# Kernel optimization log

Measured on AMD Instinct MI355X. Metric: run time of the kernel, lower is better.

Reference implementation:

```python
import jax, jax.numpy as jnp
import numpy as np

SOFTCAP = 50.0
EPS = 1e-6
N_HEADS, D_HEAD = 16, 64


def _rms(x, w):
    return x * jax.lax.rsqrt(jnp.mean(x * x, axis=-1, keepdims=True) + EPS) * w


def _rope(x, cos, sin):
    # Faithful to source: apply_rope uses x.size(1) as the position axis, but is
    # called on (B, H, T, Dh) tensors, so positions are indexed by HEAD index.
    n = x.shape[1]
    x1, x2 = x[..., 0::2], x[..., 1::2]
    c = cos[:n][None, :, None, :]
    s = sin[:n][None, :, None, :]
    return jnp.stack([x1 * c - x2 * s, x1 * s + x2 * c], axis=-1).reshape(x.shape)


def setup_inputs() -> dict:
    key = jax.random.key(0)
    ks = jax.random.split(key, 12)
    L, D, H, Dh, Dff, V, B, T = 6, 1024, N_HEADS, D_HEAD, 4096, 32000, 1, 1024
    r = lambda k, shape: jax.random.normal(k, shape, dtype=jnp.float32) * 0.02
    return {
        'x': jax.random.randint(ks[0], (B, T), 0, V, dtype=jnp.int32),
        'embed': r(ks[1], (V, D)),
        'ln1': jnp.ones((L, D), jnp.float32),
        'Wq': r(ks[2], (L, H * Dh, D)),
        'Wk': r(ks[3], (L, H * Dh, D)),
        'Wv': r(ks[4], (L, H * Dh, D)),
        'Wo': r(ks[5], (L, D, H * Dh)),
        'qn': jnp.ones((L, Dh), jnp.float32),
        'kn': jnp.ones((L, Dh), jnp.float32),
        'ln2': jnp.ones((L, D), jnp.float32),
        'Wg': r(ks[6], (L, Dff, D)),
        'Wu': r(ks[7], (L, Dff, D)),
        'Wd': r(ks[8], (L, D, Dff)),
        'ln_out': jnp.ones((D,), jnp.float32),
    }


def reference(x, embed, ln1, Wq, Wk, Wv, Wo, qn, kn, ln2, Wg, Wu, Wd, ln_out):
    B, T = x.shape
    H, Dh = N_HEADS, D_HEAD
    scale = Dh ** -0.5
    # RoPE tables (theta=10000)
    freqs = 1.0 / (10000.0 ** (jnp.arange(0, Dh, 2, dtype=jnp.float32) / Dh))
    ang = jnp.arange(T, dtype=jnp.float32)[:, None] * freqs[None, :]
    cos, sin = jnp.cos(ang), jnp.sin(ang)
    mask = jnp.triu(jnp.ones((T, T), dtype=bool), k=1)  # True above diagonal

    h = embed[x]  # (B, T, D)

    def block(h, p):
        l1, wq, wk, wv, wo, qnw, knw, l2, wg, wu, wd = p
        hn = _rms(h, l1)
        q = (hn @ wq.T).reshape(B, T, H, Dh).transpose(0, 2, 1, 3)  # (B,H,T,Dh)
        k = (hn @ wk.T).reshape(B, T, H, Dh).transpose(0, 2, 1, 3)
        v = (hn @ wv.T).reshape(B, T, H, Dh).transpose(0, 2, 1, 3)
        q = _rope(_rms(q, qnw), cos, sin)
        k = _rope(_rms(k, knw), cos, sin)
        scores = jnp.einsum('bhtd,bhsd->bhts', q, k) * scale
        scores = SOFTCAP * jnp.tanh(scores / SOFTCAP)
        scores = jnp.where(mask[None, None], -jnp.inf, scores)
        attn = jax.nn.softmax(scores, axis=-1)
        o = jnp.einsum('bhts,bhsd->bhtd', attn, v)
        o = o.transpose(0, 2, 1, 3).reshape(B, T, H * Dh)
        h = h + o @ wo.T
        hn2 = _rms(h, l2)
        h = h + (jax.nn.silu(hn2 @ wg.T) * (hn2 @ wu.T)) @ wd.T
        return h, None

    h, _ = jax.lax.scan(block, h, (ln1, Wq, Wk, Wv, Wo, qn, kn, ln2, Wg, Wu, Wd))
    # tied embed/head
    logits = _rms(h, ln_out) @ embed.T  # (B, T, V)
    return logits
```

## Files before the change

### kernel.cpp

```cpp
#include <hip/hip_runtime.h>
#include <math.h>
#include <type_traits>

typedef __bf16 bf16_t;
typedef bf16_t bf16x4 __attribute__((ext_vector_type(4)));
typedef bf16_t bf16x8 __attribute__((ext_vector_type(8)));
typedef float  f32x4  __attribute__((ext_vector_type(4)));

#define RMS_EPS 1e-6f

enum { EP_STORE = 0, EP_RESID = 1, EP_SPLIT = 2, EP_SILU = 3, EP_QKV = 4 };

template<int V> using IC = std::integral_constant<int, V>;

static __device__ __forceinline__ f32x4 mfma16(bf16x8 a, bf16x8 b, f32x4 c) {
    return __builtin_amdgcn_mfma_f32_16x16x32_bf16(a, b, c, 0, 0, 0);
}

#define GLDS(gp, lp) __builtin_amdgcn_global_load_lds( \
    (const __attribute__((address_space(1))) void*)(gp), \
    (__attribute__((address_space(3))) void*)(lp), 16, 0, 0)

template<int N> static __device__ __forceinline__ void vmwait() {
    if constexpr (N == 0)      asm volatile("s_waitcnt vmcnt(0)" ::: "memory");
    else if constexpr (N == 2) asm volatile("s_waitcnt vmcnt(2)" ::: "memory");
    else if constexpr (N == 3) asm volatile("s_waitcnt vmcnt(3)" ::: "memory");
    else if constexpr (N == 4) asm volatile("s_waitcnt vmcnt(4)" ::: "memory");
    else if constexpr (N == 6) asm volatile("s_waitcnt vmcnt(6)" ::: "memory");
    else if constexpr (N == 8) asm volatile("s_waitcnt vmcnt(8)" ::: "memory");
    __builtin_amdgcn_sched_barrier(0);
}
static __device__ __forceinline__ void bar() { __builtin_amdgcn_s_barrier(); }
static __device__ __forceinline__ void lgkm0() {
    asm volatile("s_waitcnt lgkmcnt(0)" ::: "memory");
    __builtin_amdgcn_sched_barrier(0);
}

template<int BM, int BN, int WR, int WC, int PLANES, int EPIL, int MINW, int DEPTH>
__global__ __launch_bounds__(WR * WC * 64, MINW)
void gemm_bf16(const bf16_t* __restrict__ Ah, const bf16_t* __restrict__ Al,
               const bf16_t* __restrict__ Bh,
               float* __restrict__ Cf, bf16_t* __restrict__ Ch, bf16_t* __restrict__ Cl,
               int K, int lda, int ldb, int ldc, long long sC,
               const float* __restrict__ qnw, const float* __restrict__ knw)
{
    constexpr int ASZ = BM * 32, BSZ = BN * 32;
    constexpr int NW = WR * WC;
    constexpr int NLD = (BM / 16 * (PLANES >= 2 ? 2 : 1) + BN / 16) / NW;
    __shared__ __align__(16) bf16_t sAh[DEPTH][ASZ], sBh[DEPTH][BSZ];
    __shared__ __align__(16) bf16_t sAl[PLANES >= 2 ? DEPTH : 1][PLANES >= 2 ? ASZ : 8];

    const int gx = gridDim.x;
    int id = blockIdx.x + gx * blockIdx.y;
    if (gridDim.z == 1) {
        int nwg = gx * gridDim.y;
        int q = nwg >> 3, r = nwg & 7;
        int xcd = id & 7, ix = id >> 3;
        id = (xcd < r ? xcd * (q + 1) : r * (q + 1) + (xcd - r) * q) + ix;
    }
    const int bm = id % gx, bn = id / gx;
    const int row0 = bm * BM, col0 = bn * BN;

    const size_t kofs = (size_t)blockIdx.z * K;
    Ah += kofs;  Bh += kofs;
    if constexpr (PLANES >= 2) Al += kofs;

    const int tid = threadIdx.x, lane = tid & 63, wave = tid >> 6;
    const int lr = lane & 15, lg = lane >> 4;
    constexpr int WM = BM / WR, WN = BN / WC, MF = WM / 16, NF = WN / 16;
    const int wr = wave / WC, wc = wave % WC;

    f32x4 acc[MF][NF];
    #pragma unroll
    for (int m = 0; m < MF; ++m)
        #pragma unroll
        for (int n = 0; n < NF; ++n) acc[m][n] = (f32x4){0.f, 0.f, 0.f, 0.f};

    auto stage = [&](int k0, int p) {
        #pragma unroll
        for (int i = wave; i < BM / 16; i += NW) {
            int s = i * 64 + lane, rr = s >> 2, c = s & 3;
            size_t go = (size_t)(row0 + rr) * lda + k0 + ((c ^ ((rr >> 1) & 3)) << 3);
            GLDS(Ah + go, &sAh[p][i * 512]);
            if constexpr (PLANES >= 2) GLDS(Al + go, &sAl[p][i * 512]);
        }
        #pragma unroll
        for (int i = wave; i < BN / 16; i += NW) {
            int s = i * 64 + lane, rr = s >> 2, c = s & 3;
            size_t go = (size_t)(col0 + rr) * ldb + k0 + ((c ^ ((rr >> 1) & 3)) << 3);
            GLDS(Bh + go, &sBh[p][i * 512]);
        }
    };

    auto compute = [&](int p) {
        bf16x8 ahf[MF], alf[MF], bhf[NF];
        #pragma unroll
        for (int m = 0; m < MF; ++m) {
            int rr = wr * WM + m * 16 + lr;
            int by = rr * 64 + ((lg ^ ((rr >> 1) & 3)) << 4);
            ahf[m] = *(const bf16x8*)((const char*)&sAh[p][0] + by);
            if constexpr (PLANES >= 2)
                alf[m] = *(const bf16x8*)((const char*)&sAl[p][0] + by);
        }
        #pragma unroll
        for (int n = 0; n < NF; ++n) {
            int rr = wc * WN + n * 16 + lr;
            int by = rr * 64 + ((lg ^ ((rr >> 1) & 3)) << 4);
            bhf[n] = *(const bf16x8*)((const char*)&sBh[p][0] + by);
        }
        #pragma unroll
        for (int m = 0; m < MF; ++m)
            #pragma unroll
            for (int n = 0; n < NF; ++n) {
                acc[m][n] = mfma16(ahf[m], bhf[n], acc[m][n]);
                if constexpr (PLANES >= 2)
                    acc[m][n] = mfma16(alf[m], bhf[n], acc[m][n]);
            }
    };

    if constexpr (DEPTH == 3) {
        const int NC = K >> 5;
        stage(0, 0);
        stage(32, 1);
        for (int j = 0; j + 2 < NC; ++j) {
            stage(32 * (j + 2), (j + 2) % 3);
            vmwait<2 * NLD>(); bar();
            compute(j % 3);
            bar();
        }
        vmwait<NLD>(); bar();
        compute((K >> 5) >= 2 ? ((K >> 5) - 2) % 3 : 0);
        vmwait<0>(); bar();
        compute(((K >> 5) - 1) % 3);
    } else {
        stage(0, 0);
        int k0 = 32;
        for (; k0 + 32 < K; k0 += 64) {
            stage(k0, 1);
            vmwait<NLD>(); bar();
            compute(0);
            bar();
            stage(k0 + 32, 0);
            vmwait<NLD>(); bar();
            compute(1);
            bar();
        }
        stage(k0, 1);
        vmwait<NLD>(); bar();
        compute(0);
        bar();
        vmwait<0>(); bar();
        compute(1);
    }

    if constexpr (EPIL == EP_QKV) {
        const int colbase = col0 + wc * WN;
        const int typ = colbase >> 10;
        if (typ < 2) {
            const float* nw = (typ == 0) ? qnw : knw;
            const int hh = (colbase - typ * 1024) >> 6;
            constexpr float kLogF = -0.41524101186092029f;
            #pragma unroll
            for (int m = 0; m < MF; ++m)
                #pragma unroll
                for (int r = 0; r < 4; ++r) {
                    int grow = row0 + wr * WM + m * 16 + lg * 4 + r;
                    float ss = 0.f;
                    #pragma unroll
                    for (int n = 0; n < NF; ++n) {
                        float v = acc[m][n][r];
                        ss += v * v;
                    }
                    ss += __shfl_xor(ss, 1, 64);
                    ss += __shfl_xor(ss, 2, 64);
                    ss += __shfl_xor(ss, 4, 64);
                    ss += __shfl_xor(ss, 8, 64);
                    float inv = rsqrtf(ss * (1.0f / 64.0f) + RMS_EPS);
                    #pragma unroll
                    for (int n = 0; n < NF; ++n) {
                        int i = n * 16 + lr;
                        float x = acc[m][n][r] * inv * nw[i];
                        float p = __shfl_xor(x, 1, 64);
                        float f = exp2f((float)(i >> 1) * kLogF);
                        float ang = (float)hh * f;
                        float cs = cosf(ang), sn = sinf(ang);
                        float o = (lr & 1) ? (p * sn + x * cs) : (x * cs - p * sn);
                        Ch[(size_t)grow * ldc + colbase + i] = (bf16_t)o;
                    }
                }
        } else {
            bf16_t* vTh_ = Cl;
            bf16_t* vTl_ = (bf16_t*)Cf;
            const int vcb = colbase - 2048;
            #pragma unroll
            for (int m = 0; m < MF; ++m)
                #pragma unroll
                for (int n = 0; n < NF; ++n) {
                    int vc = vcb + n * 16 + lr;
                    int grow0 = row0 + wr * WM + m * 16 + lg * 4;
                    bf16x4 hv, lv;
                    #pragma unroll
                    for (int r = 0; r < 4; ++r) {
                        float v = acc[m][n][r];
                        bf16_t hb = (bf16_t)v;
                        hv[r] = hb;
                        lv[r] = (bf16_t)(v - (float)hb);
                    }
                    *(bf16x4*)&vTh_[(size_t)vc * 1024 + grow0] = hv;
                    *(bf16x4*)&vTl_[(size_t)vc * 1024 + grow0] = lv;
                }
        }
        return;
    }

    #pragma unroll
    for (int m = 0; m < MF; ++m)
        #pragma unroll
        for (int n = 0; n < NF; ++n)
            #pragma unroll
            for (int r = 0; r < 4; ++r) {
                int grow = row0 + wr * WM + m * 16 + lg * 4 + r;
                int gcol = col0 + wc * WN + n * 16 + lr;
                float v = acc[m][n][r];
                if constexpr (EPIL == EP_SILU) {
                    float pv = __shfl_xor(v, 1, 64);
                    if (!(lr & 1)) {
                        float s = (v / (1.0f + __expf(-v))) * pv;
                        size_t off = (size_t)grow * ldc + (gcol >> 1);
                        Ch[off] = (bf16_t)s;
                    }
                } else {
                    size_t off = (size_t)blockIdx.z * sC + (size_t)grow * ldc + gcol;
                    if constexpr (EPIL == EP_STORE) {
                        Cf[off] = v;
                    } else if constexpr (EPIL == EP_RESID) {
                        Cf[off] += v;
                    } else {
                        bf16_t hb = (bf16_t)v;
                        Ch[off] = hb;
                        Cl[off] = (bf16_t)(v - (float)hb);
                    }
                }
            }
}

__global__ __launch_bounds__(512, 2)
void gemm_logits8(const bf16_t* __restrict__ Ah, const bf16_t* __restrict__ Bh,
                  float* __restrict__ Cf)
{
    constexpr int lda = 1024, ldb = 1024, ldc = 32000;
    constexpr int NT = 16;
    __shared__ __align__(16) bf16_t sA[2][2][256 * 32];
    __shared__ __align__(16) bf16_t sB[2][2][256 * 32];

    const int gx = gridDim.x;
    int id = blockIdx.x + gx * blockIdx.y;
    {
        int nwg = gx * gridDim.y;
        int q = nwg >> 3, r = nwg & 7;
        int xcd = id & 7, ix = id >> 3;
        id = (xcd < r ? xcd * (q + 1) : r * (q + 1) + (xcd - r) * q) + ix;
    }
    const int bm = id % gx, bn = id / gx;
    const int row0 = bm * 256, col0 = bn * 256;

    const int tid = threadIdx.x, lane = tid & 63, wave = tid >> 6;
    const int lr = lane & 15, lg = lane >> 4;
    const int wr = wave >> 2, wc = wave & 3;

    f32x4 acc[8][4];
    #pragma unroll
    for (int m = 0; m < 8; ++m)
        #pragma unroll
        for (int n = 0; n < 4; ++n) acc[m][n] = (f32x4){0.f, 0.f, 0.f, 0.f};

    auto stageA = [&](int chunk, int buf, int ks) {
        int k0 = chunk * 32;
        #pragma unroll
        for (int i = wave; i < 16; i += 8) {
            int s = i * 64 + lane, rr = s >> 2, c = s & 3;
            size_t go = (size_t)(row0 + rr) * lda + k0 + ((c ^ ((rr >> 1) & 3)) << 3);
            GLDS(Ah + go, &sA[buf][ks][i * 512]);
        }
    };
    auto stageB = [&](int chunk, int buf, int ks) {
        int k0 = chunk * 32;
        #pragma unroll
        for (int i = wave; i < 16; i += 8) {
            int s = i * 64 + lane, rr = s >> 2, c = s & 3;
            size_t go = (size_t)(col0 + rr) * ldb + k0 + ((c ^ ((rr >> 1) & 3)) << 3);
            GLDS(Bh + go, &sB[buf][ks][i * 512]);
        }
    };

    auto phase = [&](int t, auto ksc) {
        constexpr int ks = decltype(ksc)::value;
        const int buf = t & 1;
        bf16x8 af[8], bf4[4];
        #pragma unroll
        for (int m = 0; m < 8; ++m) {
            int rr = wr * 128 + m * 16 + lr;
            int by = rr * 64 + ((lg ^ ((rr >> 1) & 3)) << 4);
            af[m] = *(const bf16x8*)((const char*)&sA[buf][ks][0] + by);
        }
        #pragma unroll
        for (int n = 0; n < 4; ++n) {
            int rr = wc * 64 + n * 16 + lr;
            int by = rr * 64 + ((lg ^ ((rr >> 1) & 3)) << 4);
            bf4[n] = *(const bf16x8*)((const char*)&sB[buf][ks][0] + by);
        }
        if constexpr (ks == 0) {
            if (t + 1 < NT) {
                stageA(2 * (t + 1) + 1, (t + 1) & 1, 1);
                stageB(2 * (t + 1) + 1, (t + 1) & 1, 1);
                vmwait<8>();
            } else {
                vmwait<0>();
            }
        } else {
            if (t + 2 < NT) {
                stageA(2 * (t + 2), t & 1, 0);
                stageB(2 * (t + 2), t & 1, 0);
                vmwait<8>();
            } else if (t + 1 < NT) {
                vmwait<4>();
            } else {
                vmwait<0>();
            }
        }
        bar();
        lgkm0();
        __builtin_amdgcn_s_setprio(1);
        #pragma unroll
        for (int m = 0; m < 8; ++m)
            #pragma unroll
            for (int n = 0; n < 4; ++n)
                acc[m][n] = mfma16(af[m], bf4[n], acc[m][n]);
        __builtin_amdgcn_s_setprio(0);
        bar();
    };

    stageA(0, 0, 0); stageB(0, 0, 0);
    stageA(1, 0, 1); stageB(1, 0, 1);
    stageA(2, 1, 0); stageB(2, 1, 0);
    vmwait<8>(); bar();

    for (int t = 0; t < NT; ++t) {
        phase(t, IC<0>{});
        phase(t, IC<1>{});
    }

    #pragma unroll
    for (int m = 0; m < 8; ++m)
        #pragma unroll
        for (int n = 0; n < 4; ++n)
            #pragma unroll
            for (int r = 0; r < 4; ++r) {
                int grow = row0 + wr * 128 + m * 16 + lg * 4 + r;
                int gcol = col0 + wc * 64 + n * 16 + lr;
                Cf[(size_t)grow * ldc + gcol] = acc[m][n][r];
            }
}

static __device__ __forceinline__ void wsplit_body(
    int b2, int tid,
    const float* wq, const float* wk, const float* wv, const float* wo,
    const float* wg, const float* wu, const float* wd,
    bf16_t* wAh, bf16_t* wGUh, bf16_t* wdh)
{
    #pragma unroll
    for (int k = 0; k < 4; ++k) {
        int b = b2 * 4 + k;
        const float* src;
        bf16_t* dst;
        size_t so, doff;
        if (b < 4096) {
            src = b < 1024 ? wq : b < 2048 ? wk : b < 3072 ? wv : wo;
            so = (size_t)(b & 1023) * 256 + tid;
            doff = (size_t)b * 256 + tid;
            dst = wAh;
        } else if (b < 12288) {
            int bb = b - 4096;
            int row = bb < 4096 ? 2 * bb : 2 * (bb - 4096) + 1;
            src = bb < 4096 ? wg : wu;
            so = (size_t)(bb & 4095) * 256 + tid;
            doff = (size_t)row * 256 + tid;
            dst = wGUh;
        } else {
            src = wd;
            so = (size_t)(b - 12288) * 256 + tid;
            doff = so;
            dst = wdh;
        }
        f32x4 v = ((const f32x4*)src)[so];
        bf16x4 hv;
        #pragma unroll
        for (int j = 0; j < 4; ++j) hv[j] = (bf16_t)v[j];
        ((bf16x4*)dst)[doff] = hv;
    }
}

__global__ __launch_bounds__(256)
void reduce_rms_wsplit(const float* __restrict__ p, float* __restrict__ h,
                       const float* __restrict__ w, bf16_t* __restrict__ outh,
                       const float* wq, const float* wk, const float* wv,
                       const float* wo, const float* wg, const float* wu,
                       const float* wd, bf16_t* wAh, bf16_t* wGUh, bf16_t* wdh)
{
    int blk = blockIdx.x, tid = threadIdx.x;
    if (blk >= 1024) {
        if (wq) wsplit_body(blk - 1024, tid, wq, wk, wv, wo, wg, wu, wd,
                            wAh, wGUh, wdh);
        return;
    }
    size_t i = (size_t)blk * 256 + tid;
    const size_t S = (1024 * 1024) / 4;
    f32x4 a = ((const f32x4*)p)[i];
    f32x4 b = ((const f32x4*)p)[i + S];
    f32x4 c = ((const f32x4*)p)[i + 2 * S];
    f32x4 d = ((const f32x4*)p)[i + 3 * S];
    f32x4 hv = ((const f32x4*)h)[i];
    #pragma unroll
    for (int j = 0; j < 4; ++j) hv[j] += (a[j] + b[j]) + (c[j] + d[j]);
    ((f32x4*)h)[i] = hv;

    float ss = hv[0]*hv[0] + hv[1]*hv[1] + hv[2]*hv[2] + hv[3]*hv[3];
    #pragma unroll
    for (int m = 1; m < 64; m <<= 1) ss += __shfl_xor(ss, m, 64);
    __shared__ float red[4];
    if ((tid & 63) == 0) red[tid >> 6] = ss;
    __syncthreads();
    float tot = red[0] + red[1] + red[2] + red[3];
    float inv = rsqrtf(tot * (1.0f / 1024.0f) + RMS_EPS);
    f32x4 wt4 = *(const f32x4*)(w + tid * 4);
    bf16x4 hv4;
    #pragma unroll
    for (int j = 0; j < 4; ++j) hv4[j] = (bf16_t)(hv[j] * inv * wt4[j]);
    ((bf16x4*)outh)[i] = hv4;
}

__global__ __launch_bounds__(256)
void gather_rms_wsplit(const int* __restrict__ ids, const float* __restrict__ embed,
                       const float* __restrict__ w, float* __restrict__ h,
                       bf16_t* __restrict__ outh,
                       const float* wq, const float* wk, const float* wv,
                       const float* wo, const float* wg, const float* wu,
                       const float* wd, bf16_t* wAh, bf16_t* wGUh, bf16_t* wdh,
                       bf16_t* __restrict__ eh)
{
    int blk = blockIdx.x, tid = threadIdx.x;
    if (blk >= 5120) {
        int b2 = blk - 5120;
        #pragma unroll
        for (int k = 0; k < 4; ++k) {
            size_t so = ((size_t)b2 * 4 + k) * 256 + tid;
            f32x4 v = ((const f32x4*)embed)[so];
            bf16x4 hv;
            #pragma unroll
            for (int j = 0; j < 4; ++j) hv[j] = (bf16_t)v[j];
            ((bf16x4*)eh)[so] = hv;
        }
        return;
    }
    if (blk >= 1024) {
        wsplit_body(blk - 1024, tid, wq, wk, wv, wo, wg, wu, wd, wAh, wGUh, wdh);
        return;
    }
    int row = ids[blk];
    f32x4 v = ((const f32x4*)(embed + (size_t)row * 1024))[tid];
    ((f32x4*)(h + (size_t)blk * 1024))[tid] = v;

    float ss = v[0]*v[0] + v[1]*v[1] + v[2]*v[2] + v[3]*v[3];
    #pragma unroll
    for (int m = 1; m < 64; m <<= 1) ss += __shfl_xor(ss, m, 64);
    __shared__ float red[4];
    if ((tid & 63) == 0) red[tid >> 6] = ss;
    __syncthreads();
    float tot = red[0] + red[1] + red[2] + red[3];
    float inv = rsqrtf(tot * (1.0f / 1024.0f) + RMS_EPS);
    f32x4 wt4 = *(const f32x4*)(w + tid * 4);
    bf16x4 hv;
    #pragma unroll
    for (int j = 0; j < 4; ++j) hv[j] = (bf16_t)(v[j] * inv * wt4[j]);
    ((bf16x4*)outh)[(size_t)blk * 256 + tid] = hv;
}

__global__ __launch_bounds__(128, 2)
void flash_attn(const bf16_t* __restrict__ qkvh,
                const bf16_t* __restrict__ vTh, const bf16_t* __restrict__ vTl,
                bf16_t* __restrict__ oh)
{
    __shared__ __align__(16) bf16_t sQ[32*64], sK[64*64], sVh[64*64], sVl[64*64];
    __shared__ __align__(16) bf16_t sPh[32*64], sPl[32*64];

    const int q0 = blockIdx.x * 32;
    const int hh = blockIdx.y;
    const int tid = threadIdx.x, lane = tid & 63, w = tid >> 6;
    const int lr = lane & 15, lg = lane >> 4;

    #pragma unroll
    for (int ii = 0; ii < 2; ++ii) {
        int r0 = w * 16 + ii * 8;
        int r  = r0 + (lane >> 3);
        int i  = lane & 7;
        GLDS(qkvh + (size_t)(q0 + r) * 3072 + hh * 64 + ((i ^ (r & 7)) << 3),
             sQ + r0 * 64);
    }
    __syncthreads();

    bf16x8 qa[2];
    #pragma unroll
    for (int ks = 0; ks < 2; ++ks) {
        int r = w * 16 + lr;
        qa[ks] = *(const bf16x8*)((const char*)sQ + r * 128 +
                                  ((((ks << 2) | lg) ^ (r & 7)) << 4));
    }

    f32x4 o_acc[4];
    #pragma unroll
    for (int n = 0; n < 4; ++n) o_acc[n] = (f32x4){0.f, 0.f, 0.f, 0.f};
    float m_run[4] = {-1e30f, -1e30f, -1e30f, -1e30f};
    float l_run[4] = {0.f, 0.f, 0.f, 0.f};

    const int ntiles = ((q0 + 31) >> 6) + 1;
    for (int t = 0; t < ntiles; ++t) {
        const int kv0 = t * 64;
        #pragma unroll
        for (int ii = 0; ii < 4; ++ii) {
            int r0 = w * 32 + ii * 8;
            int r  = r0 + (lane >> 3);
            int i  = lane & 7;
            GLDS(qkvh + (size_t)(kv0 + r) * 3072 + 1024 + hh * 64 + ((i ^ (r & 7)) << 3),
                 sK + r0 * 64);
            GLDS(vTh + (size_t)(hh * 64 + r) * 1024 + kv0 + ((i ^ (r & 7)) << 3),
                 sVh + r0 * 64);
            GLDS(vTl + (size_t)(hh * 64 + r) * 1024 + kv0 + ((i ^ (r & 7)) << 3),
                 sVl + r0 * 64);
        }
        __syncthreads();

        f32x4 s_acc[4];
        #pragma unroll
        for (int n = 0; n < 4; ++n) s_acc[n] = (f32x4){0.f, 0.f, 0.f, 0.f};
        #pragma unroll
        for (int ks = 0; ks < 2; ++ks)
            #pragma unroll
            for (int n = 0; n < 4; ++n) {
                int r = n * 16 + lr;
                bf16x8 kb = *(const bf16x8*)((const char*)sK + r * 128 +
                                             ((((ks << 2) | lg) ^ (r & 7)) << 4));
                s_acc[n] = mfma16(qa[ks], kb, s_acc[n]);
            }

        #pragma unroll
        for (int j = 0; j < 4; ++j) {
            int qr = q0 + w * 16 + lg * 4 + j;
            float p[4];
            float mx = -1e30f;
            #pragma unroll
            for (int n = 0; n < 4; ++n) {
                float sx = s_acc[n][j] * (0.125f * 0.02f);
                float v = 50.f * (1.f - 2.f / (1.f + __expf(2.f * sx)));
                int key = kv0 + n * 16 + lr;
                if (key > qr) v = -1e30f;
                p[n] = v;
                mx = fmaxf(mx, v);
            }
            #pragma unroll
            for (int m = 1; m < 16; m <<= 1) mx = fmaxf(mx, __shfl_xor(mx, m, 64));
            float mn = fmaxf(m_run[j], mx);
            float ef = __expf(m_run[j] - mn);
            m_run[j] = mn;
            float rs = 0.f;
            #pragma unroll
            for (int n = 0; n < 4; ++n) {
                float e = __expf(p[n] - mn);
                p[n] = e;
                rs += e;
            }
            #pragma unroll
            for (int m = 1; m < 16; m <<= 1) rs += __shfl_xor(rs, m, 64);
            l_run[j] = l_run[j] * ef + rs;
            #pragma unroll
            for (int n = 0; n < 4; ++n) o_acc[n][j] *= ef;
            int r = w * 16 + lg * 4 + j;
            #pragma unroll
            for (int n = 0; n < 4; ++n) {
                int c = n * 16 + lr;
                int byo = r * 128 + ((((c >> 3) ^ (r & 7)) << 4)) + ((c & 7) << 1);
                bf16_t hb = (bf16_t)p[n];
                *(bf16_t*)((char*)sPh + byo) = hb;
                *(bf16_t*)((char*)sPl + byo) = (bf16_t)(p[n] - (float)hb);
            }
        }

        #pragma unroll
        for (int ks = 0; ks < 2; ++ks) {
            int pr = w * 16 + lr;
            int pby = pr * 128 + ((((ks << 2) | lg) ^ (pr & 7)) << 4);
            bf16x8 pa  = *(const bf16x8*)((const char*)sPh + pby);
            bf16x8 pl_ = *(const bf16x8*)((const char*)sPl + pby);
            #pragma unroll
            for (int n = 0; n < 4; ++n) {
                int vr = n * 16 + lr;
                int vby = vr * 128 + ((((ks << 2) | lg) ^ (vr & 7)) << 4);
                bf16x8 vhf = *(const bf16x8*)((const char*)sVh + vby);
                bf16x8 vlf = *(const bf16x8*)((const char*)sVl + vby);
                o_acc[n] = mfma16(pa,  vhf, o_acc[n]);
                o_acc[n] = mfma16(pl_, vhf, o_acc[n]);
                o_acc[n] = mfma16(pa,  vlf, o_acc[n]);
            }
        }
        __syncthreads();
    }

    #pragma unroll
    for (int j = 0; j < 4; ++j) {
        float inv = 1.0f / l_run[j];
        int qr = q0 + w * 16 + lg * 4 + j;
        #pragma unroll
        for (int n = 0; n < 4; ++n) {
            size_t off = (size_t)qr * 1024 + hh * 64 + n * 16 + lr;
            oh[off] = (bf16_t)(o_acc[n][j] * inv);
        }
    }
}

__global__ __launch_bounds__(256)
void rmsnorm_split(const float* __restrict__ in, const float* __restrict__ w,
                   bf16_t* __restrict__ outh)
{
    int row = blockIdx.x, tid = threadIdx.x;
    f32x4 v = *(const f32x4*)(in + (size_t)row * 1024 + tid * 4);
    float ss = v[0]*v[0] + v[1]*v[1] + v[2]*v[2] + v[3]*v[3];
    #pragma unroll
    for (int m = 1; m < 64; m <<= 1) ss += __shfl_xor(ss, m, 64);
    __shared__ float red[4];
    if ((tid & 63) == 0) red[tid >> 6] = ss;
    __syncthreads();
    float tot = red[0] + red[1] + red[2] + red[3];
    float inv = rsqrtf(tot * (1.0f / 1024.0f) + RMS_EPS);
    f32x4 wt4 = *(const f32x4*)(w + tid * 4);
    bf16x4 hv;
    #pragma unroll
    for (int j = 0; j < 4; ++j) hv[j] = (bf16_t)(v[j] * inv * wt4[j]);
    ((bf16x4*)outh)[(size_t)row * 256 + tid] = hv;
}

extern "C" void kernel_launch(void* const* d_in, const int* in_sizes, int n_in,
                              void* d_out, int out_size, void* d_ws, size_t ws_size,
                              hipStream_t stream)
{
    (void)in_sizes; (void)n_in; (void)out_size; (void)ws_size;
    const int*   x_ids = (const int*)  d_in[0];
    const float* embed = (const float*)d_in[1];
    const float* ln1   = (const float*)d_in[2];
    const float* Wq    = (const float*)d_in[3];
    const float* Wk    = (const float*)d_in[4];
    const float* Wv    = (const float*)d_in[5];
    const float* Wo    = (const float*)d_in[6];
    const float* qn    = (const float*)d_in[7];
    const float* kn    = (const float*)d_in[8];
    const float* ln2   = (const float*)d_in[9];
    const float* Wg    = (const float*)d_in[10];
    const float* Wu    = (const float*)d_in[11];
    const float* Wd    = (const float*)d_in[12];
    const float* lnout = (const float*)d_in[13];
    float* out = (float*)d_out;

    char* ws = (char*)d_ws;
    const size_t MB = 1 << 20;
    float*  h    = (float*) (ws +   0 * MB);
    bf16_t* hnh  = (bf16_t*)(ws +   4 * MB);
    bf16_t* qkvh = (bf16_t*)(ws +   8 * MB);
    bf16_t* vTh  = (bf16_t*)(ws +  20 * MB);
    bf16_t* vTl  = (bf16_t*)(ws +  22 * MB);
    bf16_t* oh   = (bf16_t*)(ws +  24 * MB);
    bf16_t* wAh  = (bf16_t*)(ws +  28 * MB);
    bf16_t* wGUh = (bf16_t*)(ws +  36 * MB);
    bf16_t* wdh  = (bf16_t*)(ws +  52 * MB);
    bf16_t* silh = (bf16_t*)(ws +  60 * MB);
    float*  wdp  = (float*) (ws +  68 * MB);
    bf16_t* eh   = (bf16_t*)(ws +  84 * MB);

    const long long M1 = 1024 * 1024;

    gather_rms_wsplit<<<13120, 256, 0, stream>>>(
        x_ids, embed, ln1, h, hnh,
        Wq, Wk, Wv, Wo, Wg, Wu, Wd, wAh, wGUh, wdh, eh);

    for (int l = 0; l < 6; ++l) {
        gemm_bf16<64,128,2,2,1,EP_QKV,4,3><<<dim3(16,24),256,0,stream>>>(
            hnh, nullptr, wAh, (float*)vTl, qkvh, vTh, 1024, 1024, 1024, 3072, 0,
            qn + l * 64, kn + l * 64);

        flash_attn<<<dim3(32,16), 128, 0, stream>>>(qkvh, vTh, vTl, oh);

        gemm_bf16<64,64,2,2,1,EP_RESID,4,3><<<dim3(16,16),256,0,stream>>>(
            oh, nullptr, wAh + 3 * M1, h, nullptr, nullptr, 1024, 1024, 1024, 1024, 0,
            nullptr, nullptr);

        rmsnorm_split<<<1024, 256, 0, stream>>>(h, ln2 + l * 1024, hnh);

        gemm_bf16<128,256,2,4,1,EP_SILU,4,3><<<dim3(8,32),512,0,stream>>>(
            hnh, nullptr, wGUh, nullptr, silh, nullptr, 1024, 1024, 1024, 4096, 0,
            nullptr, nullptr);

        gemm_bf16<128,128,2,2,1,EP_STORE,4,3><<<dim3(8,8,4),256,0,stream>>>(
            silh, nullptr, wdh, wdp, nullptr, nullptr, 1024, 4096, 4096, 1024, M1,
            nullptr, nullptr);

        const float* wnext = (l < 5) ? (ln1 + (l + 1) * 1024) : lnout;
        if (l < 5) {
            reduce_rms_wsplit<<<5120, 256, 0, stream>>>(
                wdp, h, wnext, hnh,
                Wq + (size_t)(l+1) * M1, Wk + (size_t)(l+1) * M1,
                Wv + (size_t)(l+1) * M1, Wo + (size_t)(l+1) * M1,
                Wg + (size_t)(l+1) * 4 * M1, Wu + (size_t)(l+1) * 4 * M1,
                Wd + (size_t)(l+1) * 4 * M1, wAh, wGUh, wdh);
        } else {
            reduce_rms_wsplit<<<1024, 256, 0, stream>>>(
                wdp, h, wnext, hnh,
                nullptr, nullptr, nullptr, nullptr, nullptr, nullptr, nullptr,
                wAh, wGUh, wdh);
        }
    }

    gemm_logits8<<<dim3(4,125), 512, 0, stream>>>(hnh, eh, out);
}
```

Baseline: 1.156 ms.

## Overlap next-layer weight conversion with gate/up GEMM via double-buffered weights

Next-layer fp32-to-bf16 weight conversion moves out of the reduce kernel and into extra blocks (blockIdx.z==1) of a new dedicated gate/up GEMM kernel. Double-buffered weight slots keep the conversion from overwriting weights still in use. The goal is to hide the memory-bound conversion behind the compute-bound GEMM and shrink the reduce kernel to 1024 blocks. The new GEMM uses a 128x256 tile with 3-stage LDS buffers and 4 blocks per CU in launch bounds, which may compete with the converter blocks for bandwidth and register budget.

Measured after the change: 1.125 ms. 2.7% less time.

```diff
diff --git a/kernel.cpp b/kernel.cpp
--- a/kernel.cpp
+++ b/kernel.cpp
@@ -222,24 +222,147 @@
                 int grow = row0 + wr * WM + m * 16 + lg * 4 + r;
                 int gcol = col0 + wc * WN + n * 16 + lr;
                 float v = acc[m][n][r];
-                if constexpr (EPIL == EP_SILU) {
-                    float pv = __shfl_xor(v, 1, 64);
-                    if (!(lr & 1)) {
-                        float s = (v / (1.0f + __expf(-v))) * pv;
-                        size_t off = (size_t)grow * ldc + (gcol >> 1);
-                        Ch[off] = (bf16_t)s;
-                    }
-                } else {
-                    size_t off = (size_t)blockIdx.z * sC + (size_t)grow * ldc + gcol;
-                    if constexpr (EPIL == EP_STORE) {
-                        Cf[off] = v;
-                    } else if constexpr (EPIL == EP_RESID) {
-                        Cf[off] += v;
-                    } else {
-                        bf16_t hb = (bf16_t)v;
-                        Ch[off] = hb;
-                        Cl[off] = (bf16_t)(v - (float)hb);
-                    }
+                size_t off = (size_t)blockIdx.z * sC + (size_t)grow * ldc + gcol;
+                if constexpr (EPIL == EP_STORE) {
+                    Cf[off] = v;
+                } else if constexpr (EPIL == EP_RESID) {
+                    Cf[off] += v;
+                } else if constexpr (EPIL == EP_SPLIT) {
+                    bf16_t hb = (bf16_t)v;
+                    Ch[off] = hb;
+                    Cl[off] = (bf16_t)(v - (float)hb);
+                }
+            }
+}
+
+__global__ __launch_bounds__(512, 4)
+void gemm_gu_pack(const bf16_t* __restrict__ Ah, const bf16_t* __restrict__ Bh,
+                  bf16_t* __restrict__ Ch,
+                  const float* wq, const float* wk, const float* wv,
+                  const float* wo, const float* wg, const float* wu,
+                  const float* wd, bf16_t* wAd, bf16_t* wGUd, bf16_t* wdd)
+{
+    constexpr int lda = 1024, ldb = 1024, ldc = 4096, K = 1024;
+    const int tid = threadIdx.x;
+
+    if (blockIdx.z == 1) {
+        if (!wq) return;
+        int base = ((int)blockIdx.y * 8 + (int)blockIdx.x) * 512 + tid;
+        #pragma unroll 4
+        for (int j = 0; j < 32; ++j) {
+            int v = j * 131072 + base;
+            f32x4 val;
+            bf16_t* dst;
+            size_t doff;
+            if (v < (1 << 20)) {
+                int b = v >> 8, col = v & 255;
+                const float* src = b < 1024 ? wq : b < 2048 ? wk : b < 3072 ? wv : wo;
+                val = ((const f32x4*)src)[(size_t)(b & 1023) * 256 + col];
+                dst = wAd; doff = (size_t)b * 256 + col;
+            } else if (v < 3 * (1 << 20)) {
+                int u = v - (1 << 20);
+                int bb = u >> 8, col = u & 255;
+                int row = bb < 4096 ? 2 * bb : 2 * (bb - 4096) + 1;
+                const float* src = bb < 4096 ? wg : wu;
+                val = ((const f32x4*)src)[(size_t)(bb & 4095) * 256 + col];
+                dst = wGUd; doff = (size_t)row * 256 + col;
+            } else {
+                int u = v - 3 * (1 << 20);
+                val = ((const f32x4*)wd)[u];
+                dst = wdd; doff = (size_t)u;
+            }
+            bf16x4 hv;
+            #pragma unroll
+            for (int q2 = 0; q2 < 4; ++q2) hv[q2] = (bf16_t)val[q2];
+            ((bf16x4*)dst)[doff] = hv;
+        }
+        return;
+    }
+
+    __shared__ __align__(16) bf16_t sA[3][128 * 32], sB[3][256 * 32];
+
+    int id = blockIdx.x + 8 * blockIdx.y;
+    {
+        int q = 256 >> 3;
+        int xcd = id & 7, ix = id >> 3;
+        id = xcd * q + ix;
+    }
+    const int bm = id % 8, bn = id / 8;
+    const int row0 = bm * 128, col0 = bn * 256;
+
+    const int lane = tid & 63, wave = tid >> 6;
+    const int lr = lane & 15, lg = lane >> 4;
+    const int wr = wave >> 2, wc = wave & 3;
+
+    f32x4 acc[4][4];
+    #pragma unroll
+    for (int m = 0; m < 4; ++m)
+        #pragma unroll
+        for (int n = 0; n < 4; ++n) acc[m][n] = (f32x4){0.f, 0.f, 0.f, 0.f};
+
+    auto stage = [&](int k0, int p) {
+        {
+            int i = wave;
+            int s = i * 64 + lane, rr = s >> 2, c = s & 3;
+            size_t go = (size_t)(row0 + rr) * lda + k0 + ((c ^ ((rr >> 1) & 3)) << 3);
+            GLDS(Ah + go, &sA[p][i * 512]);
+        }
+        #pragma unroll
+        for (int i = wave; i < 16; i += 8) {
+            int s = i * 64 + lane, rr = s >> 2, c = s & 3;
+            size_t go = (size_t)(col0 + rr) * ldb + k0 + ((c ^ ((rr >> 1) & 3)) << 3);
+            GLDS(Bh + go, &sB[p][i * 512]);
+        }
+    };
+
+    auto compute = [&](int p) {
+        bf16x8 af[4], bf4[4];
+        #pragma unroll
+        for (int m = 0; m < 4; ++m) {
+            int rr = wr * 64 + m * 16 + lr;
+            int by = rr * 64 + ((lg ^ ((rr >> 1) & 3)) << 4);
+            af[m] = *(const bf16x8*)((const char*)&sA[p][0] + by);
+        }
+        #pragma unroll
+        for (int n = 0; n < 4; ++n) {
+            int rr = wc * 64 + n * 16 + lr;
+            int by = rr * 64 + ((lg ^ ((rr >> 1) & 3)) << 4);
+            bf4[n] = *(const bf16x8*)((const char*)&sB[p][0] + by);
+        }
+        #pragma unroll
+        for (int m = 0; m < 4; ++m)
+            #pragma unroll
+            for (int n = 0; n < 4; ++n)
+                acc[m][n] = mfma16(af[m], bf4[n], acc[m][n]);
+    };
+
+    const int NC = K >> 5;
+    stage(0, 0);
+    stage(32, 1);
+    for (int j = 0; j + 2 < NC; ++j) {
+        stage(32 * (j + 2), (j + 2) % 3);
+        vmwait<6>(); bar();
+        compute(j % 3);
+        bar();
+    }
+    vmwait<3>(); bar();
+    compute((NC - 2) % 3);
+    vmwait<0>(); bar();
+    compute((NC - 1) % 3);
+
+    #pragma unroll
+    for (int m = 0; m < 4; ++m)
+        #pragma unroll
+        for (int n = 0; n < 4; ++n)
+            #pragma unroll
+            for (int r = 0; r < 4; ++r) {
+                int grow = row0 + wr * 64 + m * 16 + lg * 4 + r;
+                int gcol = col0 + wc * 64 + n * 16 + lr;
+                float v = acc[m][n][r];
+                float pv = __shfl_xor(v, 1, 64);
+                if (!(lr & 1)) {
+                    float s = (v / (1.0f + __expf(-v))) * pv;
+                    Ch[(size_t)grow * ldc + (gcol >> 1)] = (bf16_t)s;
                 }
             }
 }
@@ -401,18 +524,10 @@
 }
 
 __global__ __launch_bounds__(256)
-void reduce_rms_wsplit(const float* __restrict__ p, float* __restrict__ h,
-                       const float* __restrict__ w, bf16_t* __restrict__ outh,
-                       const float* wq, const float* wk, const float* wv,
-                       const float* wo, const float* wg, const float* wu,
-                       const float* wd, bf16_t* wAh, bf16_t* wGUh, bf16_t* wdh)
+void reduce_rms(const float* __restrict__ p, float* __restrict__ h,
+                const float* __restrict__ w, bf16_t* __restrict__ outh)
 {
     int blk = blockIdx.x, tid = threadIdx.x;
-    if (blk >= 1024) {
-        if (wq) wsplit_body(blk - 1024, tid, wq, wk, wv, wo, wg, wu, wd,
-                            wAh, wGUh, wdh);
-        return;
-    }
     size_t i = (size_t)blk * 256 + tid;
     const size_t S = (1024 * 1024) / 4;
     f32x4 a = ((const f32x4*)p)[i];
@@ -676,54 +791,51 @@
     bf16_t* vTh  = (bf16_t*)(ws +  20 * MB);
     bf16_t* vTl  = (bf16_t*)(ws +  22 * MB);
     bf16_t* oh   = (bf16_t*)(ws +  24 * MB);
-    bf16_t* wAh  = (bf16_t*)(ws +  28 * MB);
-    bf16_t* wGUh = (bf16_t*)(ws +  36 * MB);
-    bf16_t* wdh  = (bf16_t*)(ws +  52 * MB);
+    bf16_t* wA[2]  = {(bf16_t*)(ws +  28 * MB), (bf16_t*)(ws +  84 * MB)};
+    bf16_t* wGU[2] = {(bf16_t*)(ws +  36 * MB), (bf16_t*)(ws +  92 * MB)};
+    bf16_t* wD[2]  = {(bf16_t*)(ws +  52 * MB), (bf16_t*)(ws + 108 * MB)};
     bf16_t* silh = (bf16_t*)(ws +  60 * MB);
     float*  wdp  = (float*) (ws +  68 * MB);
-    bf16_t* eh   = (bf16_t*)(ws +  84 * MB);
+    bf16_t* eh   = (bf16_t*)(ws + 116 * MB);
 
     const long long M1 = 1024 * 1024;
 
     gather_rms_wsplit<<<13120, 256, 0, stream>>>(
         x_ids, embed, ln1, h, hnh,
-        Wq, Wk, Wv, Wo, Wg, Wu, Wd, wAh, wGUh, wdh, eh);
+        Wq, Wk, Wv, Wo, Wg, Wu, Wd, wA[0], wGU[0], wD[0], eh);
 
     for (int l = 0; l < 6; ++l) {
+        const int s = l & 1, nx = s ^ 1;
+
         gemm_bf16<64,128,2,2,1,EP_QKV,4,3><<<dim3(16,24),256,0,stream>>>(
-            hnh, nullptr, wAh, (float*)vTl, qkvh, vTh, 1024, 1024, 1024, 3072, 0,
+            hnh, nullptr, wA[s], (float*)vTl, qkvh, vTh, 1024, 1024, 1024, 3072, 0,
             qn + l * 64, kn + l * 64);
 
         flash_attn<<<dim3(32,16), 128, 0, stream>>>(qkvh, vTh, vTl, oh);
 
         gemm_bf16<64,64,2,2,1,EP_RESID,4,3><<<dim3(16,16),256,0,stream>>>(
-            oh, nullptr, wAh + 3 * M1, h, nullptr, nullptr, 1024, 1024, 1024, 1024, 0,
+            oh, nullptr, wA[s] + 3 * M1, h, nullptr, nullptr, 1024, 1024, 1024, 1024, 0,
             nullptr, nullptr);
 
         rmsnorm_split<<<1024, 256, 0, stream>>>(h, ln2 + l * 1024, hnh);
 
-        gemm_bf16<128,256,2,4,1,EP_SILU,4,3><<<dim3(8,32),512,0,stream>>>(
-            hnh, nullptr, wGUh, nullptr, silh, nullptr, 1024, 1024, 1024, 4096, 0,
+        gemm_gu_pack<<<dim3(8,32,2), 512, 0, stream>>>(
+            hnh, wGU[s], silh,
+            l < 5 ? Wq + (size_t)(l+1) * M1 : nullptr,
+            l < 5 ? Wk + (size_t)(l+1) * M1 : nullptr,
+            l < 5 ? Wv + (size_t)(l+1) * M1 : nullptr,
+            l < 5 ? Wo + (size_t)(l+1) * M1 : nullptr,
+            l < 5 ? Wg + (size_t)(l+1) * 4 * M1 : nullptr,
+            l < 5 ? Wu + (size_t)(l+1) * 4 * M1 : nullptr,
+            l < 5 ? Wd + (size_t)(l+1) * 4 * M1 : nullptr,
+            wA[nx], wGU[nx], wD[nx]);
+
+        gemm_bf16<128,128,2,2,1,EP_STORE,4,3><<<dim3(8,8,4),256,0,stream>>>(
+            silh, nullptr, wD[s], wdp, nullptr, nullptr, 1024, 4096, 4096, 1024, M1,
             nullptr, nullptr);
 
-        gemm_bf16<128,128,2,2,1,EP_STORE,4,3><<<dim3(8,8,4),256,0,stream>>>(
-            silh, nullptr, wdh, wdp, nullptr, nullptr, 1024, 4096, 4096, 1024, M1,
-            nullptr, nullptr);
-
         const float* wnext = (l < 5) ? (ln1 + (l + 1) * 1024) : lnout;
-        if (l < 5) {
-            reduce_rms_wsplit<<<5120, 256, 0, stream>>>(
-                wdp, h, wnext, hnh,
-                Wq + (size_t)(l+1) * M1, Wk + (size_t)(l+1) * M1,
-                Wv + (size_t)(l+1) * M1, Wo + (size_t)(l+1) * M1,
-                Wg + (size_t)(l+1) * 4 * M1, Wu + (size_t)(l+1) * 4 * M1,
-                Wd + (size_t)(l+1) * 4 * M1, wAh, wGUh, wdh);
-        } else {
-            reduce_rms_wsplit<<<1024, 256, 0, stream>>>(
-                wdp, h, wnext, hnh,
-                nullptr, nullptr, nullptr, nullptr, nullptr, nullptr, nullptr,
-                wAh, wGUh, wdh);
-        }
+        reduce_rms<<<1024, 256, 0, stream>>>(wdp, h, wnext, hnh);
     }
 
     gemm_logits8<<<dim3(4,125), 512, 0, stream>>>(hnh, eh, out);
```
